# Kernel optimization log

Hardware: AMD Instinct MI355X
Metric: run time of the kernel (lower is better)

Reference implementation:

```python
import jax, jax.numpy as jnp
import numpy as np
import math

B, T, C = 4, 2048, 1024
H, DQK, DV = 16, 64, 64

def setup_inputs() -> dict:
    key = jax.random.key(0)
    k1, k2, k3, k4, k5 = jax.random.split(key, 5)
    # randw(*d) = randn(*d) / sqrt(d[-1])
    x_q = jax.random.normal(k1, (B, T, C), dtype=jnp.float32)
    w_q = jax.random.normal(k2, (H, DQK, C), dtype=jnp.float32) / math.sqrt(C)
    w_k = jax.random.normal(k3, (H, DQK, C), dtype=jnp.float32) / math.sqrt(C)
    w_v = jax.random.normal(k4, (H, DV, C), dtype=jnp.float32) / math.sqrt(C)
    w_o = jax.random.normal(k5, (DV * H, C), dtype=jnp.float32) / math.sqrt(C)
    return {"x_q": x_q, "w_q": w_q, "w_k": w_k, "w_v": w_v, "w_o": w_o}

def reference(x_q, w_q, w_k, w_v, w_o):
    # self-attention: x_kv = x_q
    q = jnp.einsum('ntc,hdc->nhtd', x_q, w_q)
    k = jnp.einsum('ntc,hdc->nhtd', x_q, w_k)
    v = jnp.einsum('ntc,hdc->nhtd', x_q, w_v)
    a = jnp.einsum('nhtd,nhsd->nhts', q, k) / math.sqrt(q.shape[3])
    t = a.shape[2]
    causal_forbidden = jnp.arange(t)[:, None] < jnp.arange(t)[None, :]  # [T,S]
    a = jnp.where(causal_forbidden[None, None], -jnp.inf, a)
    a = jax.nn.softmax(a, axis=3)
    y = jnp.einsum('nhts,nhsd->nthd', a, v).reshape(a.shape[0], t, -1)
    return y @ w_o
```

## Files before the change

### kernel.cpp

```cpp
#include <hip/hip_runtime.h>
#include <stdint.h>

#define B_ 4
#define T_ 2048
#define C_ 1024
#define H_ 16
#define D_ 64
#define M_ (B_*T_)
#define K_ C_

typedef unsigned short ushort_t;
typedef __bf16 bf16x8 __attribute__((ext_vector_type(8)));
typedef float  float4_ __attribute__((ext_vector_type(4)));
typedef ushort_t ushort4_ __attribute__((ext_vector_type(4)));
typedef uint32_t uint32x2 __attribute__((ext_vector_type(2)));

__device__ __forceinline__ ushort_t f2bf(float f) {
    union { float f; uint32_t u; } c; c.f = f;
    uint32_t u = c.u;
    uint32_t r = (u + 0x7FFFu + ((u >> 16) & 1u)) >> 16;
    return (ushort_t)r;
}
__device__ __forceinline__ float4_ f4zero() { float4_ z; z[0]=0.f; z[1]=0.f; z[2]=0.f; z[3]=0.f; return z; }

__device__ __forceinline__ uint32_t cvtpk(float a, float b) {
    uint32_t r;
    asm("v_cvt_pk_bf16_f32 %0, %1, %2" : "=v"(r) : "v"(a), "v"(b));
    return r;
}

#define GLDS16(gptr, lptr) \
    __builtin_amdgcn_global_load_lds((const __attribute__((address_space(1))) uint32_t*)(gptr), \
                                     (__attribute__((address_space(3))) uint32_t*)(lptr), 16, 0, 0)

__global__ __launch_bounds__(256) void cvt_f32_bf16(const float* __restrict__ src,
                                                    ushort_t* __restrict__ dst) {
    const int i = (blockIdx.x * 256 + threadIdx.x) * 4;
    float4_ v = *(const float4_*)(src + i);
    ushort4_ o;
    #pragma unroll
    for (int e = 0; e < 4; e++) o[e] = f2bf(v[e]);
    *(ushort4_*)(dst + i) = o;
}

__global__ __launch_bounds__(256) void prep_w(const float* __restrict__ s0,
                                              const float* __restrict__ s1,
                                              const float* __restrict__ s2,
                                              ushort_t* __restrict__ dst,
                                              const float* __restrict__ wo,
                                              ushort_t* __restrict__ wot) {
    __shared__ ushort_t tile[64][65];
    const int b = blockIdx.x;
    const int tid = threadIdx.x;
    if (b < 3072) {
        const float* src = (b < 1024) ? s0 : (b < 2048) ? s1 : s2;
        const int off = (b & 1023) * 1024 + tid * 4;
        float4_ v = *(const float4_*)(src + off);
        ushort4_ o;
        #pragma unroll
        for (int e = 0; e < 4; e++) o[e] = f2bf(v[e]);
        *(ushort4_*)(dst + (size_t)b * 1024 + tid * 4) = o;
    } else {
        const int bb = b - 3072;
        const int c0 = (bb & 15) * 64;
        const int r0 = (bb >> 4) * 64;
        const int row = tid >> 2;
        const int col = (tid & 3) * 16;
        #pragma unroll
        for (int r = 0; r < 4; r++) {
            float4_ v = *(const float4_*)(wo + (size_t)(r0 + row) * 1024 + c0 + col + r * 4);
            #pragma unroll
            for (int e = 0; e < 4; e++) tile[row][col + r * 4 + e] = f2bf(v[e]);
        }
        __syncthreads();
        #pragma unroll
        for (int r = 0; r < 2; r++) {
            bf16x8 v;
            #pragma unroll
            for (int e = 0; e < 8; e++) v[e] = __builtin_bit_cast(__bf16, tile[col + r * 8 + e][row]);
            *(bf16x8*)(wot + (size_t)(c0 + row) * 1024 + r0 + col + r * 8) = v;
        }
    }
}

template<int MODE>
__global__ __launch_bounds__(256)
void gemm_bt(const ushort_t* __restrict__ A,
             const ushort_t* __restrict__ Bt,
             ushort_t* __restrict__ q_ws, ushort_t* __restrict__ k_ws,
             ushort_t* __restrict__ vt_ws, float* __restrict__ outp)
{
    __shared__ __align__(16) ushort_t As[128 * 32];
    __shared__ __align__(16) ushort_t Bs[128 * 32];
    const int tid = threadIdx.x;
    const int m0 = blockIdx.x * 128;
    const int n0 = blockIdx.y * 128;

    const int L    = tid & 63;
    const int wid  = tid >> 6;
    const int wr   = (wid >> 1) * 64;
    const int wc   = (wid & 1) * 64;
    const int quad = L >> 4;
    const int lc   = L & 15;

    float4_ acc[4][4];
    #pragma unroll
    for (int i = 0; i < 4; i++)
        #pragma unroll
        for (int j = 0; j < 4; j++) acc[i][j] = f4zero();

    const int loff0 = wid * 1024 + L * 16;
    for (int k0 = 0; k0 < K_; k0 += 32) {
        __syncthreads();
        #pragma unroll
        for (int r = 0; r < 2; r++) {
            const int off = loff0 + r * 4096;
            const int row = off >> 6;
            const int col = off & 63;
            const char* ga = (const char*)A  + (size_t)(m0 + row) * (K_ * 2) + k0 * 2 + col;
            const char* gb = (const char*)Bt + (size_t)(n0 + row) * (K_ * 2) + k0 * 2 + col;
            GLDS16(ga, (char*)As + off);
            GLDS16(gb, (char*)Bs + off);
        }
        __syncthreads();
        bf16x8 af[4], bfr[4];
        #pragma unroll
        for (int i = 0; i < 4; i++) {
            const int m = wr + i * 16 + lc;
            af[i]  = *(const bf16x8*)((const char*)As + m * 64 + quad * 16);
            const int n = wc + i * 16 + lc;
            bfr[i] = *(const bf16x8*)((const char*)Bs + n * 64 + quad * 16);
        }
        #pragma unroll
        for (int i = 0; i < 4; i++)
            #pragma unroll
            for (int j = 0; j < 4; j++)
                acc[i][j] = __builtin_amdgcn_mfma_f32_16x16x32_bf16(af[i], bfr[j], acc[i][j], 0, 0, 0);
    }

    const int mat = n0 >> 10;
    const int nb  = n0 & 1023;
    if (MODE == 1) {
        #pragma unroll
        for (int i = 0; i < 4; i++)
            #pragma unroll
            for (int j = 0; j < 4; j++)
                #pragma unroll
                for (int rg = 0; rg < 4; rg++) {
                    const int mg = m0 + wr + i * 16 + quad * 4 + rg;
                    const int cg = n0 + wc + j * 16 + lc;
                    outp[(size_t)mg * 1024 + cg] = acc[i][j][rg];
                }
    } else if (mat == 2) {
        #pragma unroll
        for (int i = 0; i < 4; i++) {
            const int mg0 = m0 + wr + i * 16 + quad * 4;
            const int n = mg0 >> 11, t0 = mg0 & 2047;
            #pragma unroll
            for (int j = 0; j < 4; j++) {
                const int ln = nb + wc + j * 16 + lc;
                const int h = ln >> 6, d = ln & 63;
                const int nh = n * H_ + h;
                ushort4_ pk;
                #pragma unroll
                for (int rg = 0; rg < 4; rg++) pk[rg] = f2bf(acc[i][j][rg]);
                *(ushort4_*)(vt_ws + ((size_t)nh * 64 + d) * T_ + t0) = pk;
            }
        }
    } else {
        const float scl = (mat == 0) ? 0.18033688011112042f : 1.0f;
        ushort_t* dstp  = (mat == 0) ? q_ws : k_ws;
        #pragma unroll
        for (int i = 0; i < 4; i++)
            #pragma unroll
            for (int j = 0; j < 4; j++)
                #pragma unroll
                for (int rg = 0; rg < 4; rg++) {
                    const int mg = m0 + wr + i * 16 + quad * 4 + rg;
                    const int ln = nb + wc + j * 16 + lc;
                    const int h = ln >> 6, d = ln & 63;
                    const int n = mg >> 11, t = mg & 2047;
                    const int nh = n * H_ + h;
                    dstp[((size_t)nh * T_ + t) * 64 + d] = f2bf(acc[i][j][rg] * scl);
                }
    }
}

#define KP 72

__global__ __launch_bounds__(512)
void attn(const ushort_t* __restrict__ q_ws, const ushort_t* __restrict__ k_ws,
          const ushort_t* __restrict__ vt_ws, ushort_t* __restrict__ y_ws)
{
    __shared__ __align__(16) ushort_t Ks[2][64 * 64];
    __shared__ __align__(16) ushort_t Vs[2][64 * 64];
    __shared__ __align__(16) ushort_t Ps[8][16 * KP];
    const int tid  = threadIdx.x;
    const int L    = tid & 63;
    const int w    = tid >> 6;
    const int quad = L >> 4, lc = L & 15;
    const int bid  = blockIdx.x;
    const int qt   = 15 - (bid >> 6);
    const int nh   = bid & 63;
    const int n    = nh >> 4;
    const int tq0  = qt * 128 + w * 16;
    const int tg   = tq0 + lc;
    const int nt   = 2 * qt + 2;
    const int dstile = tq0 >> 6;

    const ushort_t* qbase = q_ws + ((size_t)nh * T_ + tq0) * 64;
    const bf16x8 qf0 = *(const bf16x8*)(qbase + (size_t)lc * 64 + quad * 8);
    const bf16x8 qf1 = *(const bf16x8*)(qbase + (size_t)lc * 64 + quad * 8 + 32);

    float m_i = -1e30f, l_i = 0.f;
    float4_ o[4];
    #pragma unroll
    for (int r = 0; r < 4; r++) o[r] = f4zero();

    const char* kbase = (const char*)(k_ws  + (size_t)nh * T_ * 64);
    const char* vbase = (const char*)(vt_ws + (size_t)nh * 64 * T_);
    char* pwr = (char*)Ps[w] + lc * (KP * 2);

    const int ldsoff = tid * 16;
    const int srow   = ldsoff >> 7;
    const int sslot  = (ldsoff >> 4) & 7;
    const int sgs    = sslot ^ (srow & 7);
    const size_t kgo = (size_t)srow * 128 + sgs * 16;
    const size_t vgo = (size_t)srow * (T_ * 2) + sgs * 16;

    int off16[4][2];
    #pragma unroll
    for (int b = 0; b < 4; b++) {
        const int row = b * 16 + lc;
        const int r7  = lc & 7;
        off16[b][0] = row * 128 + ((quad ^ r7) << 4);
        off16[b][1] = row * 128 + (((quad + 4) ^ r7) << 4);
    }

    auto STAGE = [&](int st, int b) {
        GLDS16(kbase + (size_t)st * 8192 + kgo, (char*)Ks[b] + ldsoff);
        GLDS16(vbase + (size_t)st * 128  + vgo, (char*)Vs[b] + ldsoff);
    };

    STAGE(0, 0);
    __syncthreads();
    int cur = 0;

    for (int st = 0; st < nt; st++) {
        if (st + 1 < nt) STAGE(st + 1, cur ^ 1);
        if (st * 64 <= tq0 + 15) {
            const char* ks = (const char*)Ks[cur];
            const char* vs = (const char*)Vs[cur];

            float4_ s[4];
            #pragma unroll
            for (int sb = 0; sb < 4; sb++) {
                const bf16x8 kf0 = *(const bf16x8*)(ks + off16[sb][0]);
                const bf16x8 kf1 = *(const bf16x8*)(ks + off16[sb][1]);
                float4_ a = f4zero();
                a = __builtin_amdgcn_mfma_f32_16x16x32_bf16(kf0, qf0, a, 0, 0, 0);
                a = __builtin_amdgcn_mfma_f32_16x16x32_bf16(kf1, qf1, a, 0, 0, 0);
                s[sb] = a;
            }
            if (st >= dstile) {
                #pragma unroll
                for (int sb = 0; sb < 4; sb++)
                    #pragma unroll
                    for (int rg = 0; rg < 4; rg++) {
                        const int sg = st * 64 + sb * 16 + quad * 4 + rg;
                        if (sg > tg) s[sb][rg] = -1e30f;
                    }
            }
            float rm = -1e30f;
            #pragma unroll
            for (int sb = 0; sb < 4; sb++)
                #pragma unroll
                for (int rg = 0; rg < 4; rg++) rm = fmaxf(rm, s[sb][rg]);
            rm = fmaxf(rm, __shfl_xor(rm, 16));
            rm = fmaxf(rm, __shfl_xor(rm, 32));
            if (!__all(rm <= m_i + 8.f)) {
                const float mn    = fmaxf(m_i, rm);
                const float alpha = __builtin_amdgcn_exp2f(m_i - mn);
                l_i *= alpha;
                #pragma unroll
                for (int db = 0; db < 4; db++)
                    #pragma unroll
                    for (int rg = 0; rg < 4; rg++) o[db][rg] *= alpha;
                m_i = mn;
            }
            float rs = 0.f;
            #pragma unroll
            for (int sb = 0; sb < 4; sb++)
                #pragma unroll
                for (int rg = 0; rg < 4; rg++) {
                    const float p = __builtin_amdgcn_exp2f(s[sb][rg] - m_i);
                    s[sb][rg] = p;
                    rs += p;
                }
            rs += __shfl_xor(rs, 16);
            rs += __shfl_xor(rs, 32);
            l_i += rs;

            #pragma unroll
            for (int sb = 0; sb < 4; sb++) {
                uint32x2 pk2;
                pk2[0] = cvtpk(s[sb][0], s[sb][1]);
                pk2[1] = cvtpk(s[sb][2], s[sb][3]);
                *(uint32x2*)(pwr + sb * 32 + quad * 8) = pk2;
            }

            const bf16x8 pa0 = *(const bf16x8*)(pwr + quad * 16);
            const bf16x8 pa1 = *(const bf16x8*)(pwr + 64 + quad * 16);
            #pragma unroll
            for (int db = 0; db < 4; db++) {
                const bf16x8 vf0 = *(const bf16x8*)(vs + off16[db][0]);
                const bf16x8 vf1 = *(const bf16x8*)(vs + off16[db][1]);
                o[db] = __builtin_amdgcn_mfma_f32_16x16x32_bf16(vf0, pa0, o[db], 0, 0, 0);
                o[db] = __builtin_amdgcn_mfma_f32_16x16x32_bf16(vf1, pa1, o[db], 0, 0, 0);
            }
        }
        __syncthreads();
        cur ^= 1;
    }

    const int h = nh & 15;
    const float inv = 1.f / l_i;
    ushort_t* yrow = y_ws + ((size_t)(n * T_ + tg)) * 1024 + h * 64;
    #pragma unroll
    for (int db = 0; db < 4; db++) {
        uint32x2 pk2;
        pk2[0] = cvtpk(o[db][0] * inv, o[db][1] * inv);
        pk2[1] = cvtpk(o[db][2] * inv, o[db][3] * inv);
        *(uint32x2*)(yrow + db * 16 + quad * 4) = pk2;
    }
}

extern "C" void kernel_launch(void* const* d_in, const int* in_sizes, int n_in,
                              void* d_out, int out_size, void* d_ws, size_t ws_size,
                              hipStream_t stream) {
    (void)in_sizes; (void)n_in; (void)out_size; (void)ws_size;
    const float* x  = (const float*)d_in[0];
    const float* wq = (const float*)d_in[1];
    const float* wk = (const float*)d_in[2];
    const float* wv = (const float*)d_in[3];
    const float* wo = (const float*)d_in[4];
    char* ws = (char*)d_ws;
    const size_t MB = (size_t)1024 * 1024;
    ushort_t* x_bf  = (ushort_t*)(ws);
    ushort_t* q_ws  = (ushort_t*)(ws + 16 * MB);
    ushort_t* k_ws  = (ushort_t*)(ws + 32 * MB);
    ushort_t* vt_ws = (ushort_t*)(ws + 48 * MB);
    ushort_t* wcat  = (ushort_t*)(ws + 64 * MB);
    ushort_t* wot   = (ushort_t*)(ws + 70 * MB);
    ushort_t* y_ws  = x_bf;
    float*    outp  = (float*)d_out;

    cvt_f32_bf16<<<dim3(8192), dim3(256), 0, stream>>>(x, x_bf);
    prep_w<<<dim3(3328), dim3(256), 0, stream>>>(wq, wk, wv, wcat, wo, wot);
    gemm_bt<0><<<dim3(64, 24), dim3(256), 0, stream>>>(x_bf, wcat, q_ws, k_ws, vt_ws, nullptr);
    attn<<<dim3(1024), dim3(512), 0, stream>>>(q_ws, k_ws, vt_ws, y_ws);
    gemm_bt<1><<<dim3(64, 8), dim3(256), 0, stream>>>(y_ws, wot, nullptr, nullptr, nullptr, outp);
}
```

Baseline: 253.1 us.

## Fuse prep kernels, remap GEMM blocks per XCD, add occupancy hint

Merges the x conversion and weight preparation kernels into one launch, removing a kernel boundary. The GEMM now remaps its flat block index so consecutive blocks on the same XCD share A/B tiles, aiming to improve L2 reuse. It also adds a min-blocks-per-SM launch bound, which may constrain register allocation. The remap assumes the grid width is 64 and the block count is divisible by 8.

```diff
diff --git a/kernel.cpp b/kernel.cpp
--- a/kernel.cpp
+++ b/kernel.cpp
@@ -33,35 +33,35 @@
     __builtin_amdgcn_global_load_lds((const __attribute__((address_space(1))) uint32_t*)(gptr), \
                                      (__attribute__((address_space(3))) uint32_t*)(lptr), 16, 0, 0)
 
-__global__ __launch_bounds__(256) void cvt_f32_bf16(const float* __restrict__ src,
-                                                    ushort_t* __restrict__ dst) {
-    const int i = (blockIdx.x * 256 + threadIdx.x) * 4;
-    float4_ v = *(const float4_*)(src + i);
-    ushort4_ o;
-    #pragma unroll
-    for (int e = 0; e < 4; e++) o[e] = f2bf(v[e]);
-    *(ushort4_*)(dst + i) = o;
-}
-
-__global__ __launch_bounds__(256) void prep_w(const float* __restrict__ s0,
-                                              const float* __restrict__ s1,
-                                              const float* __restrict__ s2,
-                                              ushort_t* __restrict__ dst,
-                                              const float* __restrict__ wo,
-                                              ushort_t* __restrict__ wot) {
+__global__ __launch_bounds__(256) void prep_all(const float* __restrict__ x,
+                                                ushort_t* __restrict__ x_bf,
+                                                const float* __restrict__ s0,
+                                                const float* __restrict__ s1,
+                                                const float* __restrict__ s2,
+                                                ushort_t* __restrict__ dst,
+                                                const float* __restrict__ wo,
+                                                ushort_t* __restrict__ wot) {
     __shared__ ushort_t tile[64][65];
     const int b = blockIdx.x;
     const int tid = threadIdx.x;
-    if (b < 3072) {
-        const float* src = (b < 1024) ? s0 : (b < 2048) ? s1 : s2;
-        const int off = (b & 1023) * 1024 + tid * 4;
+    if (b < 8192) {
+        const int i = b * 1024 + tid * 4;
+        float4_ v = *(const float4_*)(x + i);
+        ushort4_ o;
+        #pragma unroll
+        for (int e = 0; e < 4; e++) o[e] = f2bf(v[e]);
+        *(ushort4_*)(x_bf + i) = o;
+    } else if (b < 11264) {
+        const int bw = b - 8192;
+        const float* src = (bw < 1024) ? s0 : (bw < 2048) ? s1 : s2;
+        const int off = (bw & 1023) * 1024 + tid * 4;
         float4_ v = *(const float4_*)(src + off);
         ushort4_ o;
         #pragma unroll
         for (int e = 0; e < 4; e++) o[e] = f2bf(v[e]);
-        *(ushort4_*)(dst + (size_t)b * 1024 + tid * 4) = o;
+        *(ushort4_*)(dst + (size_t)bw * 1024 + tid * 4) = o;
     } else {
-        const int bb = b - 3072;
+        const int bb = b - 11264;
         const int c0 = (bb & 15) * 64;
         const int r0 = (bb >> 4) * 64;
         const int row = tid >> 2;
@@ -84,7 +84,7 @@
 }
 
 template<int MODE>
-__global__ __launch_bounds__(256)
+__global__ __launch_bounds__(256, 4)
 void gemm_bt(const ushort_t* __restrict__ A,
              const ushort_t* __restrict__ Bt,
              ushort_t* __restrict__ q_ws, ushort_t* __restrict__ k_ws,
@@ -93,8 +93,11 @@
     __shared__ __align__(16) ushort_t As[128 * 32];
     __shared__ __align__(16) ushort_t Bs[128 * 32];
     const int tid = threadIdx.x;
-    const int m0 = blockIdx.x * 128;
-    const int n0 = blockIdx.y * 128;
+    const int NB   = gridDim.x * gridDim.y;
+    const int flat = blockIdx.y * gridDim.x + blockIdx.x;
+    const int fl2  = (flat & 7) * (NB >> 3) + (flat >> 3);
+    const int m0 = (fl2 & 63) * 128;
+    const int n0 = (fl2 >> 6) * 128;
 
     const int L    = tid & 63;
     const int wid  = tid >> 6;
@@ -355,8 +358,7 @@
     ushort_t* y_ws  = x_bf;
     float*    outp  = (float*)d_out;
 
-    cvt_f32_bf16<<<dim3(8192), dim3(256), 0, stream>>>(x, x_bf);
-    prep_w<<<dim3(3328), dim3(256), 0, stream>>>(wq, wk, wv, wcat, wo, wot);
+    prep_all<<<dim3(11520), dim3(256), 0, stream>>>(x, x_bf, wq, wk, wv, wcat, wo, wot);
     gemm_bt<0><<<dim3(64, 24), dim3(256), 0, stream>>>(x_bf, wcat, q_ws, k_ws, vt_ws, nullptr);
     attn<<<dim3(1024), dim3(512), 0, stream>>>(q_ws, k_ws, vt_ws, y_ws);
     gemm_bt<1><<<dim3(64, 8), dim3(256), 0, stream>>>(y_ws, wot, nullptr, nullptr, nullptr, outp);
```

After: 256.0 us. About the same (+1.2%).
